# Performance work log

Measured on AMD Instinct MI355X. Metric: run time of the kernel, lower is better.

Reference implementation:

```python
import jax, jax.numpy as jnp
import numpy as np
import itertools

N_SUBSETS = 4
TAU = 0.1


def setup_inputs() -> dict:
    key = jax.random.key(0)
    k1, k2, k3 = jax.random.split(key, 3)
    # scale projections so exp(sim/tau) stays numerically sane (module assumes small/normalized projections)
    projections = jax.random.normal(k1, (8192, 128), dtype=jnp.float32) * 0.05
    xrecon = jax.random.normal(k2, (8192, 784), dtype=jnp.float32)
    recon_label = jax.random.normal(k3, (8192, 784), dtype=jnp.float32)
    return {"projections": projections, "xrecon": xrecon, "recon_label": recon_label}


def _joint_loss(projections, xrecon, recon_label):
    # reconstruction MSE
    recon_loss = jnp.mean(jnp.square(xrecon - recon_label))

    # ---- XNegloss (SimCLR-style with n_subsets positives per group) ----
    N, D = projections.shape
    sim = (projections @ projections.T) / TAU  # [N, N] dot similarity
    gid = jnp.arange(N) // N_SUBSETS
    pos_mask = gid[:, None] == gid[None, :]  # same-group entries are positives
    exp_sim = jnp.exp(sim)
    # original code drops positive entries exactly equal to 1 (positives[positives != 1])
    pos_sum = jnp.sum(jnp.where(pos_mask & (sim != 1.0), exp_sim, 0.0), axis=-1)
    neg_sum = jnp.sum(jnp.where(pos_mask, 0.0, exp_sim), axis=-1)
    closs = jnp.mean(-jnp.log(pos_sum / (pos_sum + neg_sum)))

    # ---- distance loss: MSE over all subset pairs within each group ----
    combi = np.array(list(itertools.combinations(range(N_SUBSETS), 2)))
    left, right = combi[:, 0], combi[:, 1]
    P = projections.reshape(N // N_SUBSETS, N_SUBSETS, D)
    # per-group mean over (pairs, D) then mean over groups == global mean (equal counts)
    dist_loss = jnp.mean(jnp.square(P[:, left] - P[:, right]))

    loss = recon_loss + closs + dist_loss
    return loss, closs, recon_loss, dist_loss


def reference(projections, xrecon, recon_label):
    return _joint_loss(projections, xrecon, recon_label)
```

## Files before the change

### kernel.cpp

```cpp
#include <hip/hip_runtime.h>
#include <hip/hip_bf16.h>
#include <stdint.h>

typedef __bf16 bf16x8 __attribute__((ext_vector_type(8)));
typedef float  f32x4  __attribute__((ext_vector_type(4)));

#define NROWS   8192
#define DIMK    128
#define RECON_N 6422528
#define NTOT4   1605632
#define RECON_BLOCKS 1568
#define GROUP_BLOCKS 512
#define NTILES  2080
#define K1_BLOCKS 2592
#define K2_BLOCKS 2592

#define WS_RS     0
#define WS_G      8192
#define WS_E      16384
#define WS_RPART  24576
#define WS_DPART  26144
#define WS_PB     26656

__device__ __forceinline__ void async16(const void* g, void* l) {
    __builtin_amdgcn_global_load_lds(
        (const __attribute__((address_space(1))) void*)g,
        (__attribute__((address_space(3))) void*)l, 16, 0, 0);
}

__device__ __forceinline__ unsigned short f2bf(float f) {
    union { __hip_bfloat16 h; unsigned short u; } v;
    v.h = __float2bfloat16(f);
    return v.u;
}

__global__ __launch_bounds__(256) void stream_kernel(
        const float4* __restrict__ Pf,
        uint2* __restrict__ Pb,
        const float4* __restrict__ X,
        const float4* __restrict__ Y,
        float* __restrict__ ws) {
    __shared__ float red[4];
    const int bid = blockIdx.x;
    const int wave = threadIdx.x >> 6, lane = threadIdx.x & 63;

    if (bid < 1024) {
        int idx = bid * 256 + threadIdx.x;
        if (bid < 32) ws[WS_RS + idx] = 0.f;
        float4 a = Pf[idx];
        uint2 r;
        r.x = (uint32_t)f2bf(a.x) | ((uint32_t)f2bf(a.y) << 16);
        r.y = (uint32_t)f2bf(a.z) | ((uint32_t)f2bf(a.w) << 16);
        Pb[idx] = r;
        return;
    }

    const int idx = bid - 1024;
    int base = idx * 1024 + threadIdx.x;
    float4 a0 = X[base],       b0 = Y[base];
    float4 a1 = X[base + 256], b1 = Y[base + 256];
    float4 a2 = X[base + 512], b2 = Y[base + 512];
    float4 a3 = X[base + 768], b3 = Y[base + 768];
    float s = 0.f, d;
    d = a0.x - b0.x; s += d * d;  d = a0.y - b0.y; s += d * d;
    d = a0.z - b0.z; s += d * d;  d = a0.w - b0.w; s += d * d;
    d = a1.x - b1.x; s += d * d;  d = a1.y - b1.y; s += d * d;
    d = a1.z - b1.z; s += d * d;  d = a1.w - b1.w; s += d * d;
    d = a2.x - b2.x; s += d * d;  d = a2.y - b2.y; s += d * d;
    d = a2.z - b2.z; s += d * d;  d = a2.w - b2.w; s += d * d;
    d = a3.x - b3.x; s += d * d;  d = a3.y - b3.y; s += d * d;
    d = a3.z - b3.z; s += d * d;  d = a3.w - b3.w; s += d * d;
#pragma unroll
    for (int mm = 1; mm < 64; mm <<= 1) s += __shfl_xor(s, mm, 64);
    if (lane == 0) red[wave] = s;
    __syncthreads();
    if (threadIdx.x == 0)
        ws[WS_RPART + idx] = red[0] + red[1] + red[2] + red[3];
}

__global__ __launch_bounds__(256, 3) void sim_kernel(
        const unsigned short* __restrict__ Pb,
        const float* __restrict__ Pf,
        float* __restrict__ ws) {
    __shared__ unsigned short tile[128 * 128];
    __shared__ float sred[2][2][64];
    __shared__ float cred[2][128];
    __shared__ float dred[4];
    const int bx = blockIdx.x;
    const int wave = threadIdx.x >> 6, lane = threadIdx.x & 63;

    int role, idx;
    if (bx < 2560) {
        int r5 = bx % 5, c5 = bx / 5;
        if (r5 == 4) { role = 1; idx = c5; }
        else         { role = 0; idx = c5 * 4 + r5; }
    } else {
        role = 0; idx = 2048 + (bx - 2560);
    }

    if (role == 0) {
        float* RS = ws + WS_RS;
        float ff = 64.5f - sqrtf(64.5f * 64.5f - 2.0f * (float)idx);
        int I = (int)ff;
        int base = I * 64 - (I * (I - 1)) / 2;
        if (idx < base) { --I; base = I * 64 - (I * (I - 1)) / 2; }
        else { int nb = (I + 1) * 64 - ((I + 1) * I) / 2;
               if (idx >= nb) { ++I; base = nb; } }
        const int J = I + (idx - base);

        const int wr = wave >> 1, wc = wave & 1;
        const int m = lane & 15, kq = lane >> 4;

        const char* gB = (const char*)(Pb + (size_t)J * 128 * DIMK);
#pragma unroll
        for (int i = 0; i < 8; ++i) {
            int chunk = i * 256 + wave * 64 + lane;
            int r = chunk >> 4, qp = chunk & 15;
            async16(gB + r * 256 + (((qp - r) & 15) << 4),
                    (char*)tile + chunk * 16);
        }

        bf16x8 Af[4][4];
        const unsigned short* gA = Pb + (size_t)(I * 128 + wr * 64) * DIMK;
#pragma unroll
        for (int i = 0; i < 4; ++i) {
            const unsigned short* rowp = gA + (size_t)(i * 16 + m) * DIMK + kq * 8;
#pragma unroll
            for (int kk = 0; kk < 4; ++kk)
                Af[i][kk] = *(const bf16x8*)(rowp + kk * 32);
        }

        float rowAcc[4][4];
        float colAcc[4];
#pragma unroll
        for (int i = 0; i < 4; ++i)
#pragma unroll
            for (int r = 0; r < 4; ++r) rowAcc[i][r] = 0.f;

        __syncthreads();

#pragma unroll
        for (int j = 0; j < 4; ++j) {
            int rl = wc * 64 + j * 16 + m;
            bf16x8 Bf[4];
#pragma unroll
            for (int kk = 0; kk < 4; ++kk)
                Bf[kk] = *(const bf16x8*)((const char*)tile + rl * 256 +
                                          (((kq + kk * 4 + rl) & 15) << 4));
            f32x4 acc[4];
#pragma unroll
            for (int i = 0; i < 4; ++i) acc[i] = (f32x4){0.f, 0.f, 0.f, 0.f};
#pragma unroll
            for (int kk = 0; kk < 4; ++kk)
#pragma unroll
                for (int i = 0; i < 4; ++i)
                    acc[i] = __builtin_amdgcn_mfma_f32_16x16x32_bf16(
                        Af[i][kk], Bf[kk], acc[i], 0, 0, 0);
            float cs = 0.f;
#pragma unroll
            for (int i = 0; i < 4; ++i)
#pragma unroll
                for (int r = 0; r < 4; ++r) {
                    float e = __builtin_amdgcn_exp2f(acc[i][r] * 14.426950408889634f);
                    rowAcc[i][r] += e;
                    cs += e;
                }
            cs += __shfl_xor(cs, 16, 64);
            cs += __shfl_xor(cs, 32, 64);
            colAcc[j] = cs;
        }

#pragma unroll
        for (int i = 0; i < 4; ++i)
#pragma unroll
            for (int r = 0; r < 4; ++r) {
                float sv = rowAcc[i][r];
                sv += __shfl_xor(sv, 1, 64);
                sv += __shfl_xor(sv, 2, 64);
                sv += __shfl_xor(sv, 4, 64);
                sv += __shfl_xor(sv, 8, 64);
                rowAcc[i][r] = sv;
            }
        if (m == 0) {
#pragma unroll
            for (int i = 0; i < 4; ++i)
#pragma unroll
                for (int r = 0; r < 4; ++r)
                    sred[wc][wr][i * 16 + kq * 4 + r] = rowAcc[i][r];
        }
        if (kq == 0) {
#pragma unroll
            for (int j = 0; j < 4; ++j)
                cred[wr][wc * 64 + j * 16 + m] = colAcc[j];
        }
        __syncthreads();
        if (wc == 0) {
            float v = sred[0][wr][lane] + sred[1][wr][lane];
            atomicAdd(&RS[I * 128 + wr * 64 + lane], v);
        } else if (I != J) {
            int col = wr * 64 + lane;
            float v = cred[0][col] + cred[1][col];
            atomicAdd(&RS[J * 128 + col], v);
        }
    } else {
        float* G = ws + WS_G;
        float* E = ws + WS_E;
        int g = idx * 4 + wave;
        const float* base = Pf + (size_t)g * 4 * DIMK;
        float v[4][2];
#pragma unroll
        for (int r = 0; r < 4; ++r) {
            v[r][0] = base[r * DIMK + lane];
            v[r][1] = base[r * DIMK + 64 + lane];
        }
        float dmat[4][4];
#pragma unroll
        for (int r = 0; r < 4; ++r)
#pragma unroll
            for (int s2 = r; s2 < 4; ++s2) {
                float p = v[r][0] * v[s2][0] + v[r][1] * v[s2][1];
#pragma unroll
                for (int mm = 1; mm < 64; mm <<= 1) p += __shfl_xor(p, mm, 64);
                dmat[r][s2] = p; dmat[s2][r] = p;
            }
        if (lane == 0) {
            float distp = 0.f;
#pragma unroll
            for (int r = 0; r < 4; ++r)
#pragma unroll
                for (int s2 = r + 1; s2 < 4; ++s2)
                    distp += dmat[r][r] + dmat[s2][s2] - 2.f * dmat[r][s2];
            dred[wave] = distp;
#pragma unroll
            for (int r = 0; r < 4; ++r) {
                float Gs = 0.f, Es = 0.f;
#pragma unroll
                for (int s2 = 0; s2 < 4; ++s2) {
                    float sim = dmat[r][s2] * 10.0f;
                    float e = __expf(sim);
                    Gs += e;
                    if (sim == 1.0f) Es += e;
                }
                G[g * 4 + r] = Gs;
                E[g * 4 + r] = Es;
            }
        }
        __syncthreads();
        if (threadIdx.x == 0)
            ws[WS_DPART + idx] = dred[0] + dred[1] + dred[2] + dred[3];
    }
}

__global__ __launch_bounds__(1024) void finalize_kernel(const float* __restrict__ ws,
                                                        float* __restrict__ out) {
    __shared__ float redc[16], redr[16], redd[16];
    const float* RS = ws + WS_RS;
    const float* G  = ws + WS_G;
    const float* E  = ws + WS_E;

    float c = 0.f;
    for (int r = threadIdx.x; r < NROWS; r += 1024) {
        float Sv = RS[r];
        c += __logf(Sv - E[r]) - __logf(G[r] - E[r]);
    }
    float rs = 0.f;
    for (int i = threadIdx.x; i < RECON_BLOCKS; i += 1024) rs += ws[WS_RPART + i];
    float ds = 0.f;
    for (int i = threadIdx.x; i < GROUP_BLOCKS; i += 1024) ds += ws[WS_DPART + i];

#pragma unroll
    for (int mm = 1; mm < 64; mm <<= 1) {
        c  += __shfl_xor(c,  mm, 64);
        rs += __shfl_xor(rs, mm, 64);
        ds += __shfl_xor(ds, mm, 64);
    }
    int wave = threadIdx.x >> 6, lane = threadIdx.x & 63;
    if (lane == 0) { redc[wave] = c; redr[wave] = rs; redd[wave] = ds; }
    __syncthreads();
    if (threadIdx.x == 0) {
        float cs = 0.f, rss = 0.f, dss = 0.f;
#pragma unroll
        for (int i = 0; i < 16; ++i) { cs += redc[i]; rss += redr[i]; dss += redd[i]; }
        float closs = cs / (float)NROWS;
        float recon = rss / (float)RECON_N;
        float dist  = dss / (float)(2048 * 6 * DIMK);
        out[0] = recon + closs + dist;
        out[1] = closs;
        out[2] = recon;
        out[3] = dist;
    }
}

extern "C" void kernel_launch(void* const* d_in, const int* in_sizes, int n_in,
                              void* d_out, int out_size, void* d_ws, size_t ws_size,
                              hipStream_t stream) {
    const float* P  = (const float*)d_in[0];
    const float4* X = (const float4*)d_in[1];
    const float4* Y = (const float4*)d_in[2];
    float* out = (float*)d_out;
    float* w = (float*)d_ws;
    unsigned short* Pb = (unsigned short*)(w + WS_PB);

    stream_kernel<<<K1_BLOCKS, 256, 0, stream>>>((const float4*)P, (uint2*)Pb,
                                                 X, Y, w);
    sim_kernel<<<K2_BLOCKS, 256, 0, stream>>>(Pb, P, w);
    finalize_kernel<<<1, 1024, 0, stream>>>(w, out);
}
```

Before: 121.6 us.

## Enlarge similarity tiles to 256x128 with 512-thread blocks sharing each B tile

The similarity kernel now uses 512-thread blocks that each cover 256 rows against one 128-column B tile kept in LDS. Each staged tile is therefore reused by twice as many waves, and the launch needs about half as many blocks. The triangular tile enumeration is rewritten for the 256-row granularity, so diagonal 256x256 blocks are computed in full and skip the column-sum atomics. Off-diagonal column sums are reduced across four waves before a single atomic. The group-loss role also processes 8 groups per block. The cost is some redundant work on diagonal blocks and higher per-block register and LDS pressure under the new launch bounds.

```diff
diff --git a/kernel.cpp b/kernel.cpp
--- a/kernel.cpp
+++ b/kernel.cpp
@@ -8,12 +8,10 @@
 #define NROWS   8192
 #define DIMK    128
 #define RECON_N 6422528
-#define NTOT4   1605632
 #define RECON_BLOCKS 1568
-#define GROUP_BLOCKS 512
-#define NTILES  2080
+#define NTILES  1056
 #define K1_BLOCKS 2592
-#define K2_BLOCKS 2592
+#define K2_BLOCKS 1312
 
 #define WS_RS     0
 #define WS_G      8192
@@ -78,50 +76,50 @@
         ws[WS_RPART + idx] = red[0] + red[1] + red[2] + red[3];
 }
 
-__global__ __launch_bounds__(256, 3) void sim_kernel(
+__global__ __launch_bounds__(512, 4) void sim_kernel(
         const unsigned short* __restrict__ Pb,
         const float* __restrict__ Pf,
         float* __restrict__ ws) {
     __shared__ unsigned short tile[128 * 128];
-    __shared__ float sred[2][2][64];
-    __shared__ float cred[2][128];
-    __shared__ float dred[4];
+    __shared__ float sred[2][4][64];
+    __shared__ float cred[4][128];
+    __shared__ float dred[8];
     const int bx = blockIdx.x;
     const int wave = threadIdx.x >> 6, lane = threadIdx.x & 63;
 
     int role, idx;
-    if (bx < 2560) {
+    if (bx < 1280) {
         int r5 = bx % 5, c5 = bx / 5;
         if (r5 == 4) { role = 1; idx = c5; }
         else         { role = 0; idx = c5 * 4 + r5; }
     } else {
-        role = 0; idx = 2048 + (bx - 2560);
+        role = 0; idx = 1024 + (bx - 1280);
     }
 
     if (role == 0) {
         float* RS = ws + WS_RS;
-        float ff = 64.5f - sqrtf(64.5f * 64.5f - 2.0f * (float)idx);
+        float ff = (65.0f - sqrtf(4225.0f - 4.0f * (float)idx)) * 0.5f;
         int I = (int)ff;
-        int base = I * 64 - (I * (I - 1)) / 2;
-        if (idx < base) { --I; base = I * 64 - (I * (I - 1)) / 2; }
-        else { int nb = (I + 1) * 64 - ((I + 1) * I) / 2;
+        int base = 65 * I - I * I;
+        if (idx < base) { --I; base = 65 * I - I * I; }
+        else { int nb = 65 * (I + 1) - (I + 1) * (I + 1);
                if (idx >= nb) { ++I; base = nb; } }
-        const int J = I + (idx - base);
+        const int J = 2 * I + (idx - base);
 
         const int wr = wave >> 1, wc = wave & 1;
         const int m = lane & 15, kq = lane >> 4;
 
         const char* gB = (const char*)(Pb + (size_t)J * 128 * DIMK);
 #pragma unroll
-        for (int i = 0; i < 8; ++i) {
-            int chunk = i * 256 + wave * 64 + lane;
+        for (int i = 0; i < 4; ++i) {
+            int chunk = i * 512 + threadIdx.x;
             int r = chunk >> 4, qp = chunk & 15;
             async16(gB + r * 256 + (((qp - r) & 15) << 4),
                     (char*)tile + chunk * 16);
         }
 
         bf16x8 Af[4][4];
-        const unsigned short* gA = Pb + (size_t)(I * 128 + wr * 64) * DIMK;
+        const unsigned short* gA = Pb + (size_t)(I * 256 + wr * 64) * DIMK;
 #pragma unroll
         for (int i = 0; i < 4; ++i) {
             const unsigned short* rowp = gA + (size_t)(i * 16 + m) * DIMK + kq * 8;
@@ -196,16 +194,16 @@
         __syncthreads();
         if (wc == 0) {
             float v = sred[0][wr][lane] + sred[1][wr][lane];
-            atomicAdd(&RS[I * 128 + wr * 64 + lane], v);
-        } else if (I != J) {
-            int col = wr * 64 + lane;
-            float v = cred[0][col] + cred[1][col];
+            atomicAdd(&RS[I * 256 + wr * 64 + lane], v);
+        } else if (J >= 2 * I + 2 && (wave == 1 || wave == 3)) {
+            int col = (wave >> 1) * 64 + lane;
+            float v = cred[0][col] + cred[1][col] + cred[2][col] + cred[3][col];
             atomicAdd(&RS[J * 128 + col], v);
         }
     } else {
         float* G = ws + WS_G;
         float* E = ws + WS_E;
-        int g = idx * 4 + wave;
+        int g = idx * 8 + wave;
         const float* base = Pf + (size_t)g * 4 * DIMK;
         float v[4][2];
 #pragma unroll
@@ -246,8 +244,12 @@
             }
         }
         __syncthreads();
-        if (threadIdx.x == 0)
-            ws[WS_DPART + idx] = dred[0] + dred[1] + dred[2] + dred[3];
+        if (threadIdx.x == 0) {
+            float dd = 0.f;
+#pragma unroll
+            for (int i = 0; i < 8; ++i) dd += dred[i];
+            ws[WS_DPART + idx] = dd;
+        }
     }
 }
 
@@ -266,7 +268,7 @@
     float rs = 0.f;
     for (int i = threadIdx.x; i < RECON_BLOCKS; i += 1024) rs += ws[WS_RPART + i];
     float ds = 0.f;
-    for (int i = threadIdx.x; i < GROUP_BLOCKS; i += 1024) ds += ws[WS_DPART + i];
+    for (int i = threadIdx.x; i < 256; i += 1024) ds += ws[WS_DPART + i];
 
 #pragma unroll
     for (int mm = 1; mm < 64; mm <<= 1) {
@@ -303,6 +305,6 @@
 
     stream_kernel<<<K1_BLOCKS, 256, 0, stream>>>((const float4*)P, (uint2*)Pb,
                                                  X, Y, w);
-    sim_kernel<<<K2_BLOCKS, 256, 0, stream>>>(Pb, P, w);
+    sim_kernel<<<K2_BLOCKS, 512, 0, stream>>>(Pb, P, w);
     finalize_kernel<<<1, 1024, 0, stream>>>(w, out);
 }
```

Result: slower. 125.0 us (+2.8%).

## Enlarge symmetric Gram tiles to 256x256 with two-pass B staging

Applied to the files above, without the earlier changes.

Enlarges the upper-triangular similarity tiles from 128x128 to 256x256, so 528 tiles replace 2080. Each block holds 256 A rows in registers across four waves and streams the B half-tiles through shared memory in two passes. This cuts redundant A/B loads, block count and atomic traffic, but leaves fewer blocks for the GPU, serializes the two B loads, and changes how blocks interleave with the group-role blocks.

```diff
diff --git a/kernel.cpp b/kernel.cpp
--- a/kernel.cpp
+++ b/kernel.cpp
@@ -8,12 +8,10 @@
 #define NROWS   8192
 #define DIMK    128
 #define RECON_N 6422528
-#define NTOT4   1605632
 #define RECON_BLOCKS 1568
-#define GROUP_BLOCKS 512
-#define NTILES  2080
+#define NTILES  528
 #define K1_BLOCKS 2592
-#define K2_BLOCKS 2592
+#define K2_BLOCKS 1040
 
 #define WS_RS     0
 #define WS_G      8192
@@ -83,45 +81,42 @@
         const float* __restrict__ Pf,
         float* __restrict__ ws) {
     __shared__ unsigned short tile[128 * 128];
-    __shared__ float sred[2][2][64];
-    __shared__ float cred[2][128];
+    __shared__ float sred[4][64];
+    __shared__ float cred[4][128];
     __shared__ float dred[4];
     const int bx = blockIdx.x;
     const int wave = threadIdx.x >> 6, lane = threadIdx.x & 63;
 
     int role, idx;
-    if (bx < 2560) {
-        int r5 = bx % 5, c5 = bx / 5;
-        if (r5 == 4) { role = 1; idx = c5; }
-        else         { role = 0; idx = c5 * 4 + r5; }
-    } else {
-        role = 0; idx = 2048 + (bx - 2560);
-    }
+    if (bx < 1024) { role = bx & 1; idx = bx >> 1; }
+    else           { role = 0; idx = 512 + (bx - 1024); }
 
     if (role == 0) {
         float* RS = ws + WS_RS;
-        float ff = 64.5f - sqrtf(64.5f * 64.5f - 2.0f * (float)idx);
+        float ff = 32.5f - sqrtf(1056.25f - 2.0f * (float)idx);
         int I = (int)ff;
-        int base = I * 64 - (I * (I - 1)) / 2;
-        if (idx < base) { --I; base = I * 64 - (I * (I - 1)) / 2; }
-        else { int nb = (I + 1) * 64 - ((I + 1) * I) / 2;
+        int base = 32 * I - (I * (I - 1)) / 2;
+        if (idx < base) { --I; base = 32 * I - (I * (I - 1)) / 2; }
+        else { int nb = 32 * (I + 1) - ((I + 1) * I) / 2;
                if (idx >= nb) { ++I; base = nb; } }
         const int J = I + (idx - base);
 
-        const int wr = wave >> 1, wc = wave & 1;
         const int m = lane & 15, kq = lane >> 4;
-
-        const char* gB = (const char*)(Pb + (size_t)J * 128 * DIMK);
-#pragma unroll
-        for (int i = 0; i < 8; ++i) {
-            int chunk = i * 256 + wave * 64 + lane;
-            int r = chunk >> 4, qp = chunk & 15;
-            async16(gB + r * 256 + (((qp - r) & 15) << 4),
-                    (char*)tile + chunk * 16);
+        const int wr = wave;
+
+        {
+            const char* gB = (const char*)(Pb + (size_t)(J * 256) * DIMK);
+#pragma unroll
+            for (int i = 0; i < 8; ++i) {
+                int chunk = i * 256 + threadIdx.x;
+                int r = chunk >> 4, qp = chunk & 15;
+                async16(gB + r * 256 + (((qp - r) & 15) << 4),
+                        (char*)tile + chunk * 16);
+            }
         }
 
         bf16x8 Af[4][4];
-        const unsigned short* gA = Pb + (size_t)(I * 128 + wr * 64) * DIMK;
+        const unsigned short* gA = Pb + (size_t)(I * 256 + wr * 64) * DIMK;
 #pragma unroll
         for (int i = 0; i < 4; ++i) {
             const unsigned short* rowp = gA + (size_t)(i * 16 + m) * DIMK + kq * 8;
@@ -131,43 +126,67 @@
         }
 
         float rowAcc[4][4];
-        float colAcc[4];
 #pragma unroll
         for (int i = 0; i < 4; ++i)
 #pragma unroll
             for (int r = 0; r < 4; ++r) rowAcc[i][r] = 0.f;
 
-        __syncthreads();
-
-#pragma unroll
-        for (int j = 0; j < 4; ++j) {
-            int rl = wc * 64 + j * 16 + m;
-            bf16x8 Bf[4];
-#pragma unroll
-            for (int kk = 0; kk < 4; ++kk)
-                Bf[kk] = *(const bf16x8*)((const char*)tile + rl * 256 +
-                                          (((kq + kk * 4 + rl) & 15) << 4));
-            f32x4 acc[4];
-#pragma unroll
-            for (int i = 0; i < 4; ++i) acc[i] = (f32x4){0.f, 0.f, 0.f, 0.f};
-#pragma unroll
-            for (int kk = 0; kk < 4; ++kk)
+#pragma unroll
+        for (int c = 0; c < 2; ++c) {
+            __syncthreads();
+
+            float colAcc[8];
+#pragma unroll
+            for (int j = 0; j < 8; ++j) {
+                int rl = j * 16 + m;
+                bf16x8 Bf[4];
+#pragma unroll
+                for (int kk = 0; kk < 4; ++kk)
+                    Bf[kk] = *(const bf16x8*)((const char*)tile + rl * 256 +
+                                              (((kq + kk * 4 + rl) & 15) << 4));
+                f32x4 acc[4];
+#pragma unroll
+                for (int i = 0; i < 4; ++i) acc[i] = (f32x4){0.f, 0.f, 0.f, 0.f};
+#pragma unroll
+                for (int kk = 0; kk < 4; ++kk)
+#pragma unroll
+                    for (int i = 0; i < 4; ++i)
+                        acc[i] = __builtin_amdgcn_mfma_f32_16x16x32_bf16(
+                            Af[i][kk], Bf[kk], acc[i], 0, 0, 0);
+                float cs = 0.f;
 #pragma unroll
                 for (int i = 0; i < 4; ++i)
-                    acc[i] = __builtin_amdgcn_mfma_f32_16x16x32_bf16(
-                        Af[i][kk], Bf[kk], acc[i], 0, 0, 0);
-            float cs = 0.f;
-#pragma unroll
-            for (int i = 0; i < 4; ++i)
-#pragma unroll
-                for (int r = 0; r < 4; ++r) {
-                    float e = __builtin_amdgcn_exp2f(acc[i][r] * 14.426950408889634f);
-                    rowAcc[i][r] += e;
-                    cs += e;
+#pragma unroll
+                    for (int r = 0; r < 4; ++r) {
+                        float e = __builtin_amdgcn_exp2f(acc[i][r] * 14.426950408889634f);
+                        rowAcc[i][r] += e;
+                        cs += e;
+                    }
+                cs += __shfl_xor(cs, 16, 64);
+                cs += __shfl_xor(cs, 32, 64);
+                colAcc[j] = cs;
+            }
+            if (kq == 0) {
+#pragma unroll
+                for (int j = 0; j < 8; ++j)
+                    cred[wr][j * 16 + m] = colAcc[j];
+            }
+            __syncthreads();
+            if (c == 0) {
+                const char* gB = (const char*)(Pb + (size_t)(J * 256 + 128) * DIMK);
+#pragma unroll
+                for (int i = 0; i < 8; ++i) {
+                    int chunk = i * 256 + threadIdx.x;
+                    int r = chunk >> 4, qp = chunk & 15;
+                    async16(gB + r * 256 + (((qp - r) & 15) << 4),
+                            (char*)tile + chunk * 16);
                 }
-            cs += __shfl_xor(cs, 16, 64);
-            cs += __shfl_xor(cs, 32, 64);
-            colAcc[j] = cs;
+            }
+            if (I != J && wave < 2) {
+                int col = wave * 64 + lane;
+                float v = cred[0][col] + cred[1][col] + cred[2][col] + cred[3][col];
+                atomicAdd(&RS[J * 256 + c * 128 + col], v);
+            }
         }
 
 #pragma unroll
@@ -186,22 +205,10 @@
             for (int i = 0; i < 4; ++i)
 #pragma unroll
                 for (int r = 0; r < 4; ++r)
-                    sred[wc][wr][i * 16 + kq * 4 + r] = rowAcc[i][r];
-        }
-        if (kq == 0) {
-#pragma unroll
-            for (int j = 0; j < 4; ++j)
-                cred[wr][wc * 64 + j * 16 + m] = colAcc[j];
+                    sred[wr][i * 16 + kq * 4 + r] = rowAcc[i][r];
         }
         __syncthreads();
-        if (wc == 0) {
-            float v = sred[0][wr][lane] + sred[1][wr][lane];
-            atomicAdd(&RS[I * 128 + wr * 64 + lane], v);
-        } else if (I != J) {
-            int col = wr * 64 + lane;
-            float v = cred[0][col] + cred[1][col];
-            atomicAdd(&RS[J * 128 + col], v);
-        }
+        atomicAdd(&RS[I * 256 + wr * 64 + lane], sred[wr][lane]);
     } else {
         float* G = ws + WS_G;
         float* E = ws + WS_E;
@@ -266,7 +273,7 @@
     float rs = 0.f;
     for (int i = threadIdx.x; i < RECON_BLOCKS; i += 1024) rs += ws[WS_RPART + i];
     float ds = 0.f;
-    for (int i = threadIdx.x; i < GROUP_BLOCKS; i += 1024) ds += ws[WS_DPART + i];
+    for (int i = threadIdx.x; i < 512; i += 1024) ds += ws[WS_DPART + i];
 
 #pragma unroll
     for (int mm = 1; mm < 64; mm <<= 1) {
```

Result: slower. 227.4 us (+87.0%).
